# Optimization experiments

Measured on AMD Instinct MI355X. Metric: run time of the kernel, lower is better.

## Reference

```python
import jax, jax.numpy as jnp
import numpy as np

B, S, F, H, A = 2, 2048, 1024, 16, 64


def setup_inputs() -> dict:
    key = jax.random.key(0)
    ks = jax.random.split(key, 6)
    return {
        "key_input": jax.random.normal(ks[0], (B, S, F), dtype=jnp.float32),
        "query_input": jax.random.normal(ks[1], (B, S, F), dtype=jnp.float32),
        "value_input": jax.random.normal(ks[2], (B, S, F), dtype=jnp.float32),
        "q_w": jax.random.normal(ks[3], (H, F, A), dtype=jnp.float32) * (1.0 / np.sqrt(F)),
        "k_w": jax.random.normal(ks[4], (H, F, A), dtype=jnp.float32) * (1.0 / np.sqrt(F)),
        "v_w": jax.random.normal(ks[5], (H, F, A), dtype=jnp.float32) * (1.0 / np.sqrt(F)),
    }


def reference(key_input, query_input, value_input, q_w, k_w, v_w):
    attention_len = q_w.shape[-1]
    # per-head QKV projections: [B,S,F] x [H,F,A] -> [B,S,H,A]
    keys = jnp.einsum('bsf,hfa->bsha', key_input, k_w)
    queries = jnp.einsum('bsf,hfa->bsha', query_input, q_w)
    values = jnp.einsum('bsf,hfa->bsha', value_input, v_w)
    # scores: [B,H,Q,K]; NOTE: original softmaxes over dim=2 (the query axis)
    energy = jnp.einsum('bqha,bkha->bhqk', queries, keys) / jnp.sqrt(
        jnp.asarray(attention_len, dtype=queries.dtype))
    scores = jax.nn.softmax(energy, axis=2)
    # NOTE: original einsum 'bhqs,bsha->bsha' sums over q, keeps s aligned with values
    return jnp.einsum('bhqs,bsha->bsha', scores, values)
```

## Files before the change

### kernel.cpp

```cpp
#include <hip/hip_runtime.h>
#include <hip/hip_bf16.h>

typedef __bf16 bf16_t;
typedef __bf16 bf16x4 __attribute__((ext_vector_type(4)));
typedef __bf16 bf16x8 __attribute__((ext_vector_type(8)));
typedef float  f32x4  __attribute__((ext_vector_type(4)));

static constexpr int Mtot = 4096;
static constexpr int Ntot = 1024;
static constexpr int Ktot = 1024;
static constexpr int BM = 128, BN = 128, BK = 64;
static constexpr int BKP = 72;
static constexpr int NT  = Ktot / BK;

__global__ __launch_bounds__(512, 2)
void vproj_gemm_kernel(const float* __restrict__ A,
                       const float* __restrict__ W,
                       float* __restrict__ C)
{
    __shared__ bf16_t As[2][BM][BKP];
    __shared__ bf16_t Bs[2][BN][BKP];

    const int t    = threadIdx.x;
    const int lane = t & 63;
    const int wave = t >> 6;
    const int wm   = wave >> 2;
    const int wn   = wave & 3;

    const int tile = (blockIdx.x & 7) * 32 + (blockIdx.x >> 3);
    const int bx = tile & 7;
    const int by = tile >> 3;
    const int bm = by * BM;
    const int bn = bx * BN;

    const int bhead = t >> 8;
    const int brem  = t & 255;
    const int bkq   = brem >> 4;
    const int baq   = brem & 15;
    const float* const wbase = W + ((size_t)((bn >> 6) + bhead)) * (Ktot * 64)
                                 + (size_t)(bkq * 4) * 64 + baq * 4;

    f32x4 avreg[4], bvreg[4];

    auto load_tile = [&](int k0) {
#pragma unroll
        for (int r = 0; r < 4; ++r) {
            const int idx = r * 512 + t;
            const int row = idx >> 4, c4 = idx & 15;
            avreg[r] = *(const f32x4*)(A + (size_t)(bm + row) * Ktot + k0 + c4 * 4);
        }
        const float* wp = wbase + (size_t)k0 * 64;
#pragma unroll
        for (int r = 0; r < 4; ++r)
            bvreg[r] = *(const f32x4*)(wp + r * 64);
    };

    auto store_tile = [&](int buf) {
#pragma unroll
        for (int r = 0; r < 4; ++r) {
            const int idx = r * 512 + t;
            const int row = idx >> 4, c4 = idx & 15;
            bf16x4 p = {(bf16_t)avreg[r].x, (bf16_t)avreg[r].y,
                        (bf16_t)avreg[r].z, (bf16_t)avreg[r].w};
            *(bf16x4*)&As[buf][row][c4 * 4] = p;
        }
#pragma unroll
        for (int j = 0; j < 4; ++j) {
            bf16x4 p = {(bf16_t)bvreg[0][j], (bf16_t)bvreg[1][j],
                        (bf16_t)bvreg[2][j], (bf16_t)bvreg[3][j]};
            *(bf16x4*)&Bs[buf][bhead * 64 + baq * 4 + j][bkq * 4] = p;
        }
    };

    f32x4 acc[4][2];
#pragma unroll
    for (int mf = 0; mf < 4; ++mf)
#pragma unroll
        for (int nf = 0; nf < 2; ++nf) {
            f32x4 z = {0.f, 0.f, 0.f, 0.f};
            acc[mf][nf] = z;
        }

    const int lrow = lane & 15;
    const int lkb  = (lane >> 4) << 3;

    load_tile(0);
    store_tile(0);
    __syncthreads();

    for (int tI = 0; tI < NT; ++tI) {
        const int cur = tI & 1;

        if (tI + 1 < NT) load_tile((tI + 1) * BK);

#pragma unroll
        for (int kk = 0; kk < 2; ++kk) {
            bf16x8 af[4], bfr[2];
#pragma unroll
            for (int mf = 0; mf < 4; ++mf)
                af[mf] = *(const bf16x8*)&As[cur][wm * 64 + mf * 16 + lrow][kk * 32 + lkb];
#pragma unroll
            for (int nf = 0; nf < 2; ++nf)
                bfr[nf] = *(const bf16x8*)&Bs[cur][wn * 32 + nf * 16 + lrow][kk * 32 + lkb];
#pragma unroll
            for (int mf = 0; mf < 4; ++mf)
#pragma unroll
                for (int nf = 0; nf < 2; ++nf)
                    acc[mf][nf] = __builtin_amdgcn_mfma_f32_16x16x32_bf16(
                        af[mf], bfr[nf], acc[mf][nf], 0, 0, 0);
        }

        if (tI + 1 < NT) store_tile(cur ^ 1);

        __syncthreads();
    }

#pragma unroll
    for (int mf = 0; mf < 4; ++mf) {
        const int row0 = bm + wm * 64 + mf * 16 + ((lane >> 4) << 2);
#pragma unroll
        for (int nf = 0; nf < 2; ++nf) {
            const int col = bn + wn * 32 + nf * 16 + (lane & 15);
#pragma unroll
            for (int i = 0; i < 4; ++i)
                C[(size_t)(row0 + i) * Ntot + col] = acc[mf][nf][i];
        }
    }
}

extern "C" void kernel_launch(void* const* d_in, const int* in_sizes, int n_in,
                              void* d_out, int out_size, void* d_ws, size_t ws_size,
                              hipStream_t stream) {
    (void)in_sizes; (void)n_in; (void)d_ws; (void)ws_size; (void)out_size;
    const float* V  = (const float*)d_in[2];
    const float* Vw = (const float*)d_in[5];
    float* out      = (float*)d_out;

    const int nwg = (Mtot / BM) * (Ntot / BN);
    hipLaunchKernelGGL(vproj_gemm_kernel, dim3(nwg), dim3(512), 0, stream, V, Vw, out);
}
```

Before: 33.17 us.

## Split into bf16 conversion prepass plus direct-to-LDS bf16 GEMM

Adds a prepass kernel that converts the value input to bf16 and transposes and converts the weights into workspace. A second GEMM kernel then streams the bf16 tiles into LDS with global_load_lds, uses smaller 64x128 tiles across 512 workgroups, and raises wave priority around the MFMA block. This halves the bytes the GEMM reads and drops the in-kernel register conversion. In exchange it adds a second launch and an extra write and read of the converted data. The old fused kernel is kept as a fallback when workspace is too small.

```diff
diff --git a/kernel.cpp b/kernel.cpp
--- a/kernel.cpp
+++ b/kernel.cpp
@@ -6,63 +6,179 @@
 typedef __bf16 bf16x8 __attribute__((ext_vector_type(8)));
 typedef float  f32x4  __attribute__((ext_vector_type(4)));
 
+typedef __attribute__((address_space(1))) const void  gvoid_t;
+typedef __attribute__((address_space(3))) void        lvoid_t;
+
 static constexpr int Mtot = 4096;
 static constexpr int Ntot = 1024;
 static constexpr int Ktot = 1024;
-static constexpr int BM = 128, BN = 128, BK = 64;
-static constexpr int BKP = 72;
-static constexpr int NT  = Ktot / BK;
+
+
+__global__ __launch_bounds__(256)
+void prepass_kernel(const float* __restrict__ A, const float* __restrict__ W,
+                    bf16_t* __restrict__ Ab, bf16_t* __restrict__ Wt)
+{
+    __shared__ float wtile[64][65];
+    const int bid = blockIdx.x, t = threadIdx.x;
+
+    if (bid < 1024) {
+        const size_t base = (size_t)bid * 4096 + t * 4;
+#pragma unroll
+        for (int r = 0; r < 4; ++r) {
+            const size_t i = base + (size_t)r * 1024;
+            const f32x4 v = *(const f32x4*)(A + i);
+            bf16x4 p = {(bf16_t)v[0], (bf16_t)v[1], (bf16_t)v[2], (bf16_t)v[3]};
+            *(bf16x4*)(Ab + i) = p;
+        }
+    } else {
+        const int wb = bid - 1024;
+        const int head = wb >> 4;
+        const int k0 = (wb & 15) * 64;
+        const float* wsrc = W + (size_t)head * (Ktot * 64) + (size_t)k0 * 64;
+#pragma unroll
+        for (int i = 0; i < 4; ++i) {
+            const int idx = i * 256 + t;
+            const int kr = idx >> 4, a4 = (idx & 15) * 4;
+            const f32x4 v = *(const f32x4*)(wsrc + (size_t)kr * 64 + a4);
+            wtile[kr][a4 + 0] = v[0]; wtile[kr][a4 + 1] = v[1];
+            wtile[kr][a4 + 2] = v[2]; wtile[kr][a4 + 3] = v[3];
+        }
+        __syncthreads();
+#pragma unroll
+        for (int i = 0; i < 4; ++i) {
+            const int idx = i * 256 + t;
+            const int ar = idx >> 4, kc = (idx & 15) * 4;
+            bf16x4 p = {(bf16_t)wtile[kc + 0][ar], (bf16_t)wtile[kc + 1][ar],
+                        (bf16_t)wtile[kc + 2][ar], (bf16_t)wtile[kc + 3][ar]};
+            *(bf16x4*)(Wt + (size_t)(head * 64 + ar) * Ktot + k0 + kc) = p;
+        }
+    }
+}
+
+__global__ __launch_bounds__(256, 2)
+void gemm_bf16_kernel(const bf16_t* __restrict__ Ab, const bf16_t* __restrict__ Bt,
+                      float* __restrict__ C)
+{
+    __shared__ bf16_t As[2][64 * 64];
+    __shared__ bf16_t Bs[2][128 * 64];
+
+    const int t = threadIdx.x, lane = t & 63, wave = t >> 6;
+    const int wm = wave & 1, wn = wave >> 1;
+
+    const int g = (blockIdx.x & 7) * 64 + (blockIdx.x >> 3);
+    const int by = g >> 3, bx = g & 7;
+    const int bm = by * 64, bn = bx * 128;
+
+    const int lrow = lane & 15;
+    const int lkb = (lane >> 4) * 8;
+
+    f32x4 acc[2][4];
+#pragma unroll
+    for (int mf = 0; mf < 2; ++mf)
+#pragma unroll
+        for (int nf = 0; nf < 4; ++nf) {
+            f32x4 z = {0.f, 0.f, 0.f, 0.f};
+            acc[mf][nf] = z;
+        }
+
+    auto STAGE = [&](int buf, int k0) {
+#pragma unroll
+        for (int j = 0; j < 2; ++j) {
+            const int chunk = (wave * 2 + j) * 64 + lane;
+            const int row = chunk >> 3, kb = (chunk & 7) * 8;
+            const bf16_t* gp = Ab + (size_t)(bm + row) * Ktot + k0 + kb;
+            __builtin_amdgcn_global_load_lds((gvoid_t*)gp,
+                (lvoid_t*)&As[buf][(wave * 2 + j) * 512], 16, 0, 0);
+        }
+#pragma unroll
+        for (int j = 0; j < 4; ++j) {
+            const int chunk = (wave * 4 + j) * 64 + lane;
+            const int row = chunk >> 3, kb = (chunk & 7) * 8;
+            const bf16_t* gp = Bt + (size_t)(bn + row) * Ktot + k0 + kb;
+            __builtin_amdgcn_global_load_lds((gvoid_t*)gp,
+                (lvoid_t*)&Bs[buf][(wave * 4 + j) * 512], 16, 0, 0);
+        }
+    };
+
+    STAGE(0, 0);
+    __syncthreads();
+
+    constexpr int NT = Ktot / 64;
+    for (int tI = 0; tI < NT; ++tI) {
+        const int cur = tI & 1;
+        if (tI + 1 < NT) STAGE(cur ^ 1, (tI + 1) * 64);
+
+#pragma unroll
+        for (int kk = 0; kk < 2; ++kk) {
+            bf16x8 af[2], bfr[4];
+#pragma unroll
+            for (int mf = 0; mf < 2; ++mf)
+                af[mf] = *(const bf16x8*)&As[cur][(wm * 32 + mf * 16 + lrow) * 64 + kk * 32 + lkb];
+#pragma unroll
+            for (int nf = 0; nf < 4; ++nf)
+                bfr[nf] = *(const bf16x8*)&Bs[cur][(wn * 64 + nf * 16 + lrow) * 64 + kk * 32 + lkb];
+            __builtin_amdgcn_s_setprio(1);
+#pragma unroll
+            for (int mf = 0; mf < 2; ++mf)
+#pragma unroll
+                for (int nf = 0; nf < 4; ++nf)
+                    acc[mf][nf] = __builtin_amdgcn_mfma_f32_16x16x32_bf16(
+                        af[mf], bfr[nf], acc[mf][nf], 0, 0, 0);
+            __builtin_amdgcn_s_setprio(0);
+        }
+        __syncthreads();
+    }
+
+#pragma unroll
+    for (int mf = 0; mf < 2; ++mf) {
+        const int row0 = bm + wm * 32 + mf * 16 + ((lane >> 4) << 2);
+#pragma unroll
+        for (int nf = 0; nf < 4; ++nf) {
+            const int col = bn + wn * 64 + nf * 16 + (lane & 15);
+#pragma unroll
+            for (int i = 0; i < 4; ++i)
+                C[(size_t)(row0 + i) * Ntot + col] = acc[mf][nf][i];
+        }
+    }
+}
+
+static constexpr int FBM = 128, FBN = 128, FBK = 64, FBKP = 72;
 
 __global__ __launch_bounds__(512, 2)
-void vproj_gemm_kernel(const float* __restrict__ A,
-                       const float* __restrict__ W,
-                       float* __restrict__ C)
+void vproj_fused_kernel(const float* __restrict__ A, const float* __restrict__ W,
+                        float* __restrict__ C)
 {
-    __shared__ bf16_t As[2][BM][BKP];
-    __shared__ bf16_t Bs[2][BN][BKP];
-
-    const int t    = threadIdx.x;
-    const int lane = t & 63;
-    const int wave = t >> 6;
-    const int wm   = wave >> 2;
-    const int wn   = wave & 3;
-
+    __shared__ bf16_t As[2][FBM][FBKP];
+    __shared__ bf16_t Bs[2][FBN][FBKP];
+
+    const int t = threadIdx.x, lane = t & 63, wave = t >> 6;
+    const int wm = wave >> 2, wn = wave & 3;
     const int tile = (blockIdx.x & 7) * 32 + (blockIdx.x >> 3);
-    const int bx = tile & 7;
-    const int by = tile >> 3;
-    const int bm = by * BM;
-    const int bn = bx * BN;
-
-    const int bhead = t >> 8;
-    const int brem  = t & 255;
-    const int bkq   = brem >> 4;
-    const int baq   = brem & 15;
+    const int bm = (tile >> 3) * FBM, bn = (tile & 7) * FBN;
+
+    const int bhead = t >> 8, brem = t & 255;
+    const int bkq = brem >> 4, baq = brem & 15;
     const float* const wbase = W + ((size_t)((bn >> 6) + bhead)) * (Ktot * 64)
                                  + (size_t)(bkq * 4) * 64 + baq * 4;
-
     f32x4 avreg[4], bvreg[4];
 
     auto load_tile = [&](int k0) {
 #pragma unroll
         for (int r = 0; r < 4; ++r) {
             const int idx = r * 512 + t;
-            const int row = idx >> 4, c4 = idx & 15;
-            avreg[r] = *(const f32x4*)(A + (size_t)(bm + row) * Ktot + k0 + c4 * 4);
+            avreg[r] = *(const f32x4*)(A + (size_t)(bm + (idx >> 4)) * Ktot + k0 + (idx & 15) * 4);
         }
         const float* wp = wbase + (size_t)k0 * 64;
 #pragma unroll
-        for (int r = 0; r < 4; ++r)
-            bvreg[r] = *(const f32x4*)(wp + r * 64);
+        for (int r = 0; r < 4; ++r) bvreg[r] = *(const f32x4*)(wp + r * 64);
     };
-
     auto store_tile = [&](int buf) {
 #pragma unroll
         for (int r = 0; r < 4; ++r) {
             const int idx = r * 512 + t;
-            const int row = idx >> 4, c4 = idx & 15;
-            bf16x4 p = {(bf16_t)avreg[r].x, (bf16_t)avreg[r].y,
-                        (bf16_t)avreg[r].z, (bf16_t)avreg[r].w};
-            *(bf16x4*)&As[buf][row][c4 * 4] = p;
+            bf16x4 p = {(bf16_t)avreg[r][0], (bf16_t)avreg[r][1],
+                        (bf16_t)avreg[r][2], (bf16_t)avreg[r][3]};
+            *(bf16x4*)&As[buf][idx >> 4][(idx & 15) * 4] = p;
         }
 #pragma unroll
         for (int j = 0; j < 4; ++j) {
@@ -76,23 +192,14 @@
 #pragma unroll
     for (int mf = 0; mf < 4; ++mf)
 #pragma unroll
-        for (int nf = 0; nf < 2; ++nf) {
-            f32x4 z = {0.f, 0.f, 0.f, 0.f};
-            acc[mf][nf] = z;
-        }
-
-    const int lrow = lane & 15;
-    const int lkb  = (lane >> 4) << 3;
-
-    load_tile(0);
-    store_tile(0);
-    __syncthreads();
-
-    for (int tI = 0; tI < NT; ++tI) {
+        for (int nf = 0; nf < 2; ++nf) { f32x4 z = {0,0,0,0}; acc[mf][nf] = z; }
+
+    const int lrow = lane & 15, lkb = (lane >> 4) << 3;
+    load_tile(0); store_tile(0); __syncthreads();
+
+    for (int tI = 0; tI < Ktot / FBK; ++tI) {
         const int cur = tI & 1;
-
-        if (tI + 1 < NT) load_tile((tI + 1) * BK);
-
+        if (tI + 1 < Ktot / FBK) load_tile((tI + 1) * FBK);
 #pragma unroll
         for (int kk = 0; kk < 2; ++kk) {
             bf16x8 af[4], bfr[2];
@@ -109,12 +216,9 @@
                     acc[mf][nf] = __builtin_amdgcn_mfma_f32_16x16x32_bf16(
                         af[mf], bfr[nf], acc[mf][nf], 0, 0, 0);
         }
-
-        if (tI + 1 < NT) store_tile(cur ^ 1);
-
+        if (tI + 1 < Ktot / FBK) store_tile(cur ^ 1);
         __syncthreads();
     }
-
 #pragma unroll
     for (int mf = 0; mf < 4; ++mf) {
         const int row0 = bm + wm * 64 + mf * 16 + ((lane >> 4) << 2);
@@ -131,11 +235,23 @@
 extern "C" void kernel_launch(void* const* d_in, const int* in_sizes, int n_in,
                               void* d_out, int out_size, void* d_ws, size_t ws_size,
                               hipStream_t stream) {
-    (void)in_sizes; (void)n_in; (void)d_ws; (void)ws_size; (void)out_size;
+    (void)in_sizes; (void)n_in; (void)out_size;
     const float* V  = (const float*)d_in[2];
     const float* Vw = (const float*)d_in[5];
     float* out      = (float*)d_out;
 
-    const int nwg = (Mtot / BM) * (Ntot / BN);
-    hipLaunchKernelGGL(vproj_gemm_kernel, dim3(nwg), dim3(512), 0, stream, V, Vw, out);
-}
+    const size_t abBytes = (size_t)Mtot * Ktot * sizeof(bf16_t);
+    const size_t wtBytes = (size_t)Ntot * Ktot * sizeof(bf16_t);
+
+    if (ws_size >= abBytes + wtBytes) {
+        bf16_t* Ab = (bf16_t*)d_ws;
+        bf16_t* Wt = (bf16_t*)((char*)d_ws + abBytes);
+        hipLaunchKernelGGL(prepass_kernel, dim3(1024 + 256), dim3(256), 0, stream,
+                           V, Vw, Ab, Wt);
+        hipLaunchKernelGGL(gemm_bf16_kernel, dim3((Mtot / 64) * (Ntot / 128)),
+                           dim3(256), 0, stream, Ab, Wt, out);
+    } else {
+        hipLaunchKernelGGL(vproj_fused_kernel, dim3(256), dim3(512), 0, stream,
+                           V, Vw, out);
+    }
+}
```

Measured after the change: 32.62 us. Within noise of the previous version (-1.6%).

## Shrink GEMM tiles to 64x64 with swizzled LDS and more workgroups

Applied to the files above, without the earlier changes.

Retiles the V-projection GEMM from 128x128 blocks of 512 threads to 64x64 blocks of 256 threads, quadrupling the workgroup count to fill the GPU better. Shared memory padding is replaced by an XOR swizzle, global and LDS accesses are widened to 8-element vectors, and MFMA issue gets raised wave priority. The trade-off is lower operand reuse per tile, meaning more global traffic for the fp32 inputs, plus an extra barrier per k-step.

```diff
diff --git a/kernel.cpp b/kernel.cpp
--- a/kernel.cpp
+++ b/kernel.cpp
@@ -2,125 +2,129 @@
 #include <hip/hip_bf16.h>
 
 typedef __bf16 bf16_t;
-typedef __bf16 bf16x4 __attribute__((ext_vector_type(4)));
 typedef __bf16 bf16x8 __attribute__((ext_vector_type(8)));
+typedef float  f32x2  __attribute__((ext_vector_type(2)));
 typedef float  f32x4  __attribute__((ext_vector_type(4)));
 
 static constexpr int Mtot = 4096;
 static constexpr int Ntot = 1024;
 static constexpr int Ktot = 1024;
-static constexpr int BM = 128, BN = 128, BK = 64;
-static constexpr int BKP = 72;
-static constexpr int NT  = Ktot / BK;
+static constexpr int NT   = Ktot / 64;
 
-__global__ __launch_bounds__(512, 2)
-void vproj_gemm_kernel(const float* __restrict__ A,
-                       const float* __restrict__ W,
-                       float* __restrict__ C)
+__global__ __launch_bounds__(256, 4)
+void fused_vproj_kernel(const float* __restrict__ A, const float* __restrict__ W,
+                        float* __restrict__ C)
 {
-    __shared__ bf16_t As[2][BM][BKP];
-    __shared__ bf16_t Bs[2][BN][BKP];
+    __shared__ bf16_t As[2][64 * 64];
+    __shared__ bf16_t Bs[2][64 * 64];
 
-    const int t    = threadIdx.x;
-    const int lane = t & 63;
-    const int wave = t >> 6;
-    const int wm   = wave >> 2;
-    const int wn   = wave & 3;
+    const int t = threadIdx.x, lane = t & 63, wave = t >> 6;
+    const int wm = wave & 1, wn = wave >> 1;
 
-    const int tile = (blockIdx.x & 7) * 32 + (blockIdx.x >> 3);
-    const int bx = tile & 7;
-    const int by = tile >> 3;
-    const int bm = by * BM;
-    const int bn = bx * BN;
+    const int g  = (blockIdx.x & 7) * 128 + (blockIdx.x >> 3);
+    const int by = g >> 4, bx = g & 15;
+    const int bm = by * 64, bn = bx * 64;
 
-    const int bhead = t >> 8;
-    const int brem  = t & 255;
-    const int bkq   = brem >> 4;
-    const int baq   = brem & 15;
-    const float* const wbase = W + ((size_t)((bn >> 6) + bhead)) * (Ktot * 64)
-                                 + (size_t)(bkq * 4) * 64 + baq * 4;
+    const int lrow = lane & 15, lq = lane >> 4;
 
-    f32x4 avreg[4], bvreg[4];
+    const int ac = t & 31;
+    const int ko = t >> 5;
+    const float* const wbase = W + (size_t)bx * (Ktot * 64) + (size_t)(8 * ko) * 64 + 2 * ac;
 
-    auto load_tile = [&](int k0) {
+    f32x4 aA[2][2];
+    f32x2 bB[8];
+
+    auto LOAD = [&](int k0) {
 #pragma unroll
-        for (int r = 0; r < 4; ++r) {
-            const int idx = r * 512 + t;
-            const int row = idx >> 4, c4 = idx & 15;
-            avreg[r] = *(const f32x4*)(A + (size_t)(bm + row) * Ktot + k0 + c4 * 4);
+        for (int j = 0; j < 2; ++j) {
+            const int idx8 = j * 256 + t;
+            const int row = idx8 >> 3, o8 = idx8 & 7;
+            const float* ap = A + (size_t)(bm + row) * Ktot + k0 + o8 * 8;
+            aA[j][0] = *(const f32x4*)(ap);
+            aA[j][1] = *(const f32x4*)(ap + 4);
         }
         const float* wp = wbase + (size_t)k0 * 64;
 #pragma unroll
-        for (int r = 0; r < 4; ++r)
-            bvreg[r] = *(const f32x4*)(wp + r * 64);
+        for (int j = 0; j < 8; ++j)
+            bB[j] = *(const f32x2*)(wp + (size_t)j * 64);
     };
 
-    auto store_tile = [&](int buf) {
+    auto STORE = [&](int buf) {
 #pragma unroll
-        for (int r = 0; r < 4; ++r) {
-            const int idx = r * 512 + t;
-            const int row = idx >> 4, c4 = idx & 15;
-            bf16x4 p = {(bf16_t)avreg[r].x, (bf16_t)avreg[r].y,
-                        (bf16_t)avreg[r].z, (bf16_t)avreg[r].w};
-            *(bf16x4*)&As[buf][row][c4 * 4] = p;
+        for (int j = 0; j < 2; ++j) {
+            const int idx8 = j * 256 + t;
+            const int row = idx8 >> 3, o8 = idx8 & 7;
+            bf16x8 v = {(bf16_t)aA[j][0][0], (bf16_t)aA[j][0][1],
+                        (bf16_t)aA[j][0][2], (bf16_t)aA[j][0][3],
+                        (bf16_t)aA[j][1][0], (bf16_t)aA[j][1][1],
+                        (bf16_t)aA[j][1][2], (bf16_t)aA[j][1][3]};
+            *(bf16x8*)&As[buf][row * 64 + (o8 ^ (row & 7)) * 8] = v;
         }
 #pragma unroll
-        for (int j = 0; j < 4; ++j) {
-            bf16x4 p = {(bf16_t)bvreg[0][j], (bf16_t)bvreg[1][j],
-                        (bf16_t)bvreg[2][j], (bf16_t)bvreg[3][j]};
-            *(bf16x4*)&Bs[buf][bhead * 64 + baq * 4 + j][bkq * 4] = p;
+        for (int e = 0; e < 2; ++e) {
+            const int n = 2 * ac + e;
+            bf16x8 v = {(bf16_t)bB[0][e], (bf16_t)bB[1][e],
+                        (bf16_t)bB[2][e], (bf16_t)bB[3][e],
+                        (bf16_t)bB[4][e], (bf16_t)bB[5][e],
+                        (bf16_t)bB[6][e], (bf16_t)bB[7][e]};
+            *(bf16x8*)&Bs[buf][n * 64 + (ko ^ (n & 7)) * 8] = v;
         }
     };
 
-    f32x4 acc[4][2];
+    f32x4 acc[2][2];
 #pragma unroll
-    for (int mf = 0; mf < 4; ++mf)
+    for (int mf = 0; mf < 2; ++mf)
 #pragma unroll
         for (int nf = 0; nf < 2; ++nf) {
             f32x4 z = {0.f, 0.f, 0.f, 0.f};
             acc[mf][nf] = z;
         }
 
-    const int lrow = lane & 15;
-    const int lkb  = (lane >> 4) << 3;
+    auto COMPUTE = [&](int cur) {
+#pragma unroll
+        for (int kk = 0; kk < 2; ++kk) {
+            const int c16 = kk * 4 + lq;
+            bf16x8 af[2], bfr[2];
+#pragma unroll
+            for (int mf = 0; mf < 2; ++mf) {
+                const int R = wm * 32 + mf * 16 + lrow;
+                af[mf] = *(const bf16x8*)&As[cur][R * 64 + (c16 ^ (R & 7)) * 8];
+            }
+#pragma unroll
+            for (int nf = 0; nf < 2; ++nf) {
+                const int R = wn * 32 + nf * 16 + lrow;
+                bfr[nf] = *(const bf16x8*)&Bs[cur][R * 64 + (c16 ^ (R & 7)) * 8];
+            }
+            __builtin_amdgcn_s_setprio(1);
+#pragma unroll
+            for (int mf = 0; mf < 2; ++mf)
+#pragma unroll
+                for (int nf = 0; nf < 2; ++nf)
+                    acc[mf][nf] = __builtin_amdgcn_mfma_f32_16x16x32_bf16(
+                        af[mf], bfr[nf], acc[mf][nf], 0, 0, 0);
+            __builtin_amdgcn_s_setprio(0);
+        }
+    };
 
-    load_tile(0);
-    store_tile(0);
+    LOAD(0);
+    STORE(0);
     __syncthreads();
 
     for (int tI = 0; tI < NT; ++tI) {
         const int cur = tI & 1;
-
-        if (tI + 1 < NT) load_tile((tI + 1) * BK);
-
-#pragma unroll
-        for (int kk = 0; kk < 2; ++kk) {
-            bf16x8 af[4], bfr[2];
-#pragma unroll
-            for (int mf = 0; mf < 4; ++mf)
-                af[mf] = *(const bf16x8*)&As[cur][wm * 64 + mf * 16 + lrow][kk * 32 + lkb];
-#pragma unroll
-            for (int nf = 0; nf < 2; ++nf)
-                bfr[nf] = *(const bf16x8*)&Bs[cur][wn * 32 + nf * 16 + lrow][kk * 32 + lkb];
-#pragma unroll
-            for (int mf = 0; mf < 4; ++mf)
-#pragma unroll
-                for (int nf = 0; nf < 2; ++nf)
-                    acc[mf][nf] = __builtin_amdgcn_mfma_f32_16x16x32_bf16(
-                        af[mf], bfr[nf], acc[mf][nf], 0, 0, 0);
-        }
-
-        if (tI + 1 < NT) store_tile(cur ^ 1);
-
+        if (tI + 1 < NT) LOAD((tI + 1) * 64);
+        COMPUTE(cur);
+        __syncthreads();
+        if (tI + 1 < NT) STORE(cur ^ 1);
         __syncthreads();
     }
 
 #pragma unroll
-    for (int mf = 0; mf < 4; ++mf) {
-        const int row0 = bm + wm * 64 + mf * 16 + ((lane >> 4) << 2);
+    for (int mf = 0; mf < 2; ++mf) {
+        const int row0 = bm + wm * 32 + mf * 16 + (lq << 2);
 #pragma unroll
         for (int nf = 0; nf < 2; ++nf) {
-            const int col = bn + wn * 32 + nf * 16 + (lane & 15);
+            const int col = bn + wn * 32 + nf * 16 + lrow;
 #pragma unroll
             for (int i = 0; i < 4; ++i)
                 C[(size_t)(row0 + i) * Ntot + col] = acc[mf][nf][i];
@@ -136,6 +140,7 @@
     const float* Vw = (const float*)d_in[5];
     float* out      = (float*)d_out;
 
-    const int nwg = (Mtot / BM) * (Ntot / BN);
-    hipLaunchKernelGGL(vproj_gemm_kernel, dim3(nwg), dim3(512), 0, stream, V, Vw, out);
+    const int nwg = (Mtot / 64) * (Ntot / 64);
+    hipLaunchKernelGGL(fused_vproj_kernel, dim3(nwg), dim3(256), 0, stream,
+                       V, Vw, out);
 }
```

New measurement: 35.36 us. 1.07x slower.
